# Kernel optimization log

Hardware: AMD Instinct MI355X
Metric: run time of the kernel (lower is better)

Reference implementation:

```python
import jax, jax.numpy as jnp
import numpy as np

B, N, D, T = 32, 512, 128, 8
NEG_SLOPE = 0.2
MASK_VAL = -1e10


def _xavier(key, shape, gain=1.0):
    fan_in, fan_out = shape[0], int(np.prod(shape[1:]))
    limit = gain * np.sqrt(6.0 / (fan_in + fan_out))
    return jax.random.uniform(key, shape, jnp.float32, -limit, limit)


def setup_inputs() -> dict:
    key = jax.random.key(0)
    ks = jax.random.split(key, 8)
    atom_embeddings = jax.random.normal(ks[0], (B, N, D), dtype=jnp.float32)
    # bond types in [-1, T-1]; -1 = no bond (masked)
    edges = jax.random.randint(ks[1], (B, N, N), 0, T + 1, dtype=jnp.int64) - 1
    Qw = _xavier(ks[2], (D, D))
    Kw = _xavier(ks[3], (D, D))
    Vw = _xavier(ks[4], (D, D))
    Pw = _xavier(ks[5], (D, D))
    Qb = jnp.zeros((D,), jnp.float32)
    Kb = jnp.zeros((D,), jnp.float32)
    Vb = jnp.zeros((D,), jnp.float32)
    Pb = jnp.zeros((D,), jnp.float32)
    a = _xavier(ks[6], (D, D, T), gain=1.414)
    return {"atom_embeddings": atom_embeddings, "edges": edges,
            "Qw": Qw, "Qb": Qb, "Kw": Kw, "Kb": Kb, "Vw": Vw, "Vb": Vb,
            "a": a, "Pw": Pw, "Pb": Pb}


def reference(atom_embeddings, edges, Qw, Qb, Kw, Kb, Vw, Vb, a, Pw, Pb):
    # torch Linear: x @ W.T + b
    src = atom_embeddings @ Qw.T + Qb            # (B,N,D)
    dst = atom_embeddings @ Kw.T + Kb            # (B,N,D)
    val = atom_embeddings @ Vw.T + Vb            # (B,N,D)

    # bilinear edge-type scores: s[b,n,m,t] = src[b,n,:] @ a[:,:,t] @ dst[b,m,:]
    ts = jnp.einsum('bnd,det->bnet', src, a)     # (B,N,D,T)
    scores = jnp.einsum('bnet,bme->bnmt', ts, dst)  # (B,N,N,T)

    # gather the slice for each edge's bond type (clamp -1 -> 0 like torch)
    idx = jnp.clip(edges, 0, None)[..., None]    # (B,N,N,1)
    att = jnp.take_along_axis(scores, idx, axis=-1)[..., 0]  # (B,N,N)
    att = jnp.where(edges == -1, MASK_VAL, att)
    att = jnp.where(att >= 0, att, NEG_SLOPE * att)  # leaky_relu
    att = jax.nn.softmax(att, axis=-1)           # (B,N,N)

    out = att @ val                              # (B,N,D)
    return out @ Pw.T + Pb
```

## Files before the change

kernel.cpp:

```cpp
#include <hip/hip_runtime.h>
#include <stdint.h>


typedef short bf16x8 __attribute__((ext_vector_type(8)));
typedef float f32x4 __attribute__((ext_vector_type(4)));
typedef unsigned short u16;
typedef unsigned int u32;

__device__ __forceinline__ u16 f2bf(float x) {
    union { float f; u32 u; } v; v.f = x;
    u32 r = v.u + 0x7FFFu + ((v.u >> 16) & 1u);
    return (u16)(r >> 16);
}
__device__ __forceinline__ float bf2f(u16 h) {
    union { u32 u; float f; } v; v.u = ((u32)h) << 16; return v.f;
}
__device__ __forceinline__ void split_hl(float x, u16& h, u16& l) {
    h = f2bf(x);
    l = f2bf(x - bf2f(h));
}
__device__ __forceinline__ f32x4 mfma16(bf16x8 a, bf16x8 b, f32x4 c) {
    return __builtin_amdgcn_mfma_f32_16x16x32_bf16(a, b, c, 0, 0, 0);
}

__global__ void prep_kernel(const float* __restrict__ Qw, const float* __restrict__ Qb,
                            const float* __restrict__ Kw, const float* __restrict__ Kb,
                            const float* __restrict__ Vw, const float* __restrict__ Vb,
                            const float* __restrict__ Aa, const float* __restrict__ Pw,
                            u16* __restrict__ WH, u16* __restrict__ WL,
                            float* __restrict__ bcat) {
    int gid = blockIdx.x * 256 + threadIdx.x;
    if (gid >= 1280 * 128) return;
    int j = gid >> 7, d = gid & 127;
    float v, bias = 0.f;
    if (j < 128) { v = Kw[j * 128 + d]; bias = Kb[j]; }
    else if (j < 256) {
        int jj = j - 128;
        float s = 0.f, bs = 0.f;
        for (int k = 0; k < 128; k++) {
            float p = Pw[jj * 128 + k];
            s += p * Vw[k * 128 + d];
            bs += p * Vb[k];
        }
        v = s; bias = bs;
    } else {
        int r = j - 256, t = r >> 7, jj = r & 127;
        float s = 0.f, bs = 0.f;
        for (int e = 0; e < 128; e++) {
            float av = Aa[(e * 128 + jj) * 8 + t];
            s += Qw[e * 128 + d] * av;
            bs += Qb[e] * av;
        }
        v = s; bias = bs;
    }
    u16 h, l; split_hl(v, h, l);
    WH[gid] = h; WL[gid] = l;
    if (d == 0) bcat[j] = bias;
}

__global__ void detect_kernel(const int* __restrict__ E, int* __restrict__ flag) {
    __shared__ int bad;
    if (threadIdx.x == 0) bad = 0;
    __syncthreads();
    int w0 = E[2 * threadIdx.x + 1];
    int w1 = E[2 * (threadIdx.x + 256) + 1];
    if (!(w0 == 0 || w0 == -1) || !(w1 == 0 || w1 == -1)) atomicOr(&bad, 1);
    __syncthreads();
    if (threadIdx.x == 0) *flag = (bad ? 0 : 1);
}

__global__ void econv_kernel(const void* __restrict__ E, const int* __restrict__ flag,
                             signed char* __restrict__ E8) {
    int i = (blockIdx.x * 256 + threadIdx.x) * 4;
    char4 o;
    if (*flag) {
        const long long* p = (const long long*)E;
        o.x = (signed char)p[i]; o.y = (signed char)p[i + 1];
        o.z = (signed char)p[i + 2]; o.w = (signed char)p[i + 3];
    } else {
        const int* p = (const int*)E;
        o.x = (signed char)p[i]; o.y = (signed char)p[i + 1];
        o.z = (signed char)p[i + 2]; o.w = (signed char)p[i + 3];
    }
    *(char4*)(E8 + i) = o;
}

__launch_bounds__(256, 2)
__global__ void gemm1_kernel(const float* __restrict__ X,
                             const u16* __restrict__ WH, const u16* __restrict__ WL,
                             const float* __restrict__ bcat,
                             u16* __restrict__ CH, u16* __restrict__ CL,
                             u16* __restrict__ VTH, u16* __restrict__ VTL) {
    const int id = blockIdx.x;
    const int xcd = id & 7, q5 = id >> 3;
    const int g = xcd * 32 + q5 / 20;
    const int jt = q5 - (q5 / 20) * 20;
    const int j0 = jt * 64;
    const int g0 = g * 64;
    __shared__ u16 AH[64 * 128], AL[64 * 128], BH[64 * 128], BL[64 * 128];
    const int tid = threadIdx.x;
    {
        const float4* Xv = (const float4*)(X + (size_t)g0 * 128);
        #pragma unroll
        for (int i = 0; i < 8; i++) {
            int idx = tid + i * 256;
            float4 x = Xv[idx];
            int row = idx >> 5, c4 = idx & 31;
            int boff = (row * 256 + c4 * 8) ^ ((row & 7) << 4);
            u16* ph = (u16*)((char*)AH + boff);
            u16* pl = (u16*)((char*)AL + boff);
            const float* xf = (const float*)&x;
            #pragma unroll
            for (int q = 0; q < 4; q++) { u16 h, l; split_hl(xf[q], h, l); ph[q] = h; pl[q] = l; }
        }
        const uint4* bh = (const uint4*)(WH + (size_t)j0 * 128);
        const uint4* bl = (const uint4*)(WL + (size_t)j0 * 128);
        #pragma unroll
        for (int i = 0; i < 4; i++) {
            int idx = tid + i * 256;
            int row = idx >> 4, ch = idx & 15;
            int boff = (row * 256 + ch * 16) ^ ((row & 7) << 4);
            *(uint4*)((char*)BH + boff) = bh[idx];
            *(uint4*)((char*)BL + boff) = bl[idx];
        }
    }
    __syncthreads();
    const int wid = tid >> 6, lane = tid & 63;
    const int wr = (wid >> 1) * 32, wc = (wid & 1) * 32;
    const int lr = lane & 15, lg = lane >> 4;
    f32x4 acc[2][2] = {};
    #pragma unroll
    for (int ks = 0; ks < 4; ks++) {
        const int kb2 = (ks * 32 + lg * 8) * 2;
        bf16x8 afh[2], afl[2], bfh[2], bfl[2];
        #pragma unroll
        for (int r = 0; r < 2; r++) {
            int row = wr + r * 16 + lr;
            int boff = (row * 256 + kb2) ^ ((row & 7) << 4);
            afh[r] = *(const bf16x8*)((const char*)AH + boff);
            afl[r] = *(const bf16x8*)((const char*)AL + boff);
        }
        #pragma unroll
        for (int c = 0; c < 2; c++) {
            int row = wc + c * 16 + lr;
            int boff = (row * 256 + kb2) ^ ((row & 7) << 4);
            bfh[c] = *(const bf16x8*)((const char*)BH + boff);
            bfl[c] = *(const bf16x8*)((const char*)BL + boff);
        }
        #pragma unroll
        for (int r = 0; r < 2; r++)
        #pragma unroll
        for (int c = 0; c < 2; c++) {
            acc[r][c] = mfma16(afh[r], bfh[c], acc[r][c]);
            acc[r][c] = mfma16(afh[r], bfl[c], acc[r][c]);
            acc[r][c] = mfma16(afl[r], bfh[c], acc[r][c]);
        }
    }
    const bool valTile = (j0 >= 128 && j0 < 256);
    #pragma unroll
    for (int r = 0; r < 2; r++)
    #pragma unroll
    for (int c = 0; c < 2; c++) {
        int j = j0 + wc + c * 16 + lr;
        float bias = bcat[j];
        #pragma unroll
        for (int q = 0; q < 4; q++) {
            int g1 = g0 + wr + r * 16 + 4 * lg + q;
            float v = acc[r][c][q] + bias;
            u16 h, l; split_hl(v, h, l);
            if (valTile) {
                int bb = g1 >> 9, n = g1 & 511;
                size_t off = ((size_t)(bb * 128 + (j - 128))) * 512 + n;
                VTH[off] = h; VTL[off] = l;
            } else {
                size_t off = (size_t)g1 * 1280 + j;
                CH[off] = h; CL[off] = l;
            }
        }
    }
}

__launch_bounds__(512, 2)
__global__ void scores_kernel(const u16* __restrict__ CH, const u16* __restrict__ CL,
                              const signed char* __restrict__ E8,
                              float* __restrict__ att) {
    const int id = blockIdx.x;
    const int xcd = id & 7, j = id >> 3;
    const int m0 = (j & 3) * 128;
    const int pair = xcd * 32 + (j >> 2);
    const int n0 = (pair & 7) * 64, b = pair >> 3;
    __shared__ u16 BH[128 * 128], BL[128 * 128];
    __shared__ u16 AH[2][64 * 128], AL[2][64 * 128];
    const int tid = threadIdx.x;
    const int wid = tid >> 6, lane = tid & 63;
    const int wr = (wid >> 2) * 32, wc = (wid & 3) * 32;
    const int lr = lane & 15, lg = lane >> 4;

    #pragma unroll
    for (int i = 0; i < 4; i++) {
        int idx = tid + i * 512;
        int row = idx >> 4, ch = idx & 15;
        size_t src = (size_t)(b * 512 + m0 + row) * 1280;
        int boff = (row * 256 + ch * 16) ^ ((row & 7) << 4);
        *(uint4*)((char*)BH + boff) = ((const uint4*)(CH + src))[ch];
        *(uint4*)((char*)BL + boff) = ((const uint4*)(CL + src))[ch];
    }
    int ed[2][2][4];
    #pragma unroll
    for (int r = 0; r < 2; r++)
    #pragma unroll
    for (int c = 0; c < 2; c++)
    #pragma unroll
    for (int q = 0; q < 4; q++) {
        int n = n0 + wr + r * 16 + 4 * lg + q;
        int m = m0 + wc + c * 16 + lr;
        ed[r][c][q] = E8[((size_t)b * 512 + n) * 512 + m];
    }
    uint4 rh[2], rl[2];
    {
        #pragma unroll
        for (int i = 0; i < 2; i++) {
            int idx = tid + i * 512;
            int row = idx >> 4, ch = idx & 15;
            size_t src = (size_t)(b * 512 + n0 + row) * 1280 + 256;
            rh[i] = ((const uint4*)(CH + src))[ch];
            rl[i] = ((const uint4*)(CL + src))[ch];
        }
        #pragma unroll
        for (int i = 0; i < 2; i++) {
            int idx = tid + i * 512;
            int row = idx >> 4, ch = idx & 15;
            int boff = (row * 256 + ch * 16) ^ ((row & 7) << 4);
            *(uint4*)((char*)AH[0] + boff) = rh[i];
            *(uint4*)((char*)AL[0] + boff) = rl[i];
        }
    }
    __syncthreads();
    bf16x8 bfh[4][2], bfl[4][2];
    #pragma unroll
    for (int ks = 0; ks < 4; ks++) {
        const int kb2 = (ks * 32 + lg * 8) * 2;
        #pragma unroll
        for (int c = 0; c < 2; c++) {
            int row = wc + c * 16 + lr;
            int boff = (row * 256 + kb2) ^ ((row & 7) << 4);
            bfh[ks][c] = *(const bf16x8*)((const char*)BH + boff);
            bfl[ks][c] = *(const bf16x8*)((const char*)BL + boff);
        }
    }
    float sel[2][2][4];
    #pragma unroll
    for (int r = 0; r < 2; r++)
    #pragma unroll
    for (int c = 0; c < 2; c++)
    #pragma unroll
    for (int q = 0; q < 4; q++) sel[r][c][q] = 0.f;

    for (int t = 0; t < 8; t++) {
        const int cur = t & 1;
        uint4 nh[2], nl[2];
        if (t < 7) {
            #pragma unroll
            for (int i = 0; i < 2; i++) {
                int idx = tid + i * 512;
                int row = idx >> 4, ch = idx & 15;
                size_t src = (size_t)(b * 512 + n0 + row) * 1280 + 256 + (t + 1) * 128;
                nh[i] = ((const uint4*)(CH + src))[ch];
                nl[i] = ((const uint4*)(CL + src))[ch];
            }
        }
        f32x4 acc[2][2] = {};
        #pragma unroll
        for (int ks = 0; ks < 4; ks++) {
            const int kb2 = (ks * 32 + lg * 8) * 2;
            bf16x8 afh[2], afl[2];
            #pragma unroll
            for (int r = 0; r < 2; r++) {
                int row = wr + r * 16 + lr;
                int boff = (row * 256 + kb2) ^ ((row & 7) << 4);
                afh[r] = *(const bf16x8*)((const char*)AH[cur] + boff);
                afl[r] = *(const bf16x8*)((const char*)AL[cur] + boff);
            }
            #pragma unroll
            for (int r = 0; r < 2; r++)
            #pragma unroll
            for (int c = 0; c < 2; c++) {
                acc[r][c] = mfma16(afh[r], bfh[ks][c], acc[r][c]);
                acc[r][c] = mfma16(afh[r], bfl[ks][c], acc[r][c]);
                acc[r][c] = mfma16(afl[r], bfh[ks][c], acc[r][c]);
            }
        }
        #pragma unroll
        for (int r = 0; r < 2; r++)
        #pragma unroll
        for (int c = 0; c < 2; c++)
        #pragma unroll
        for (int q = 0; q < 4; q++) {
            int ec = ed[r][c][q] < 0 ? 0 : ed[r][c][q];
            sel[r][c][q] = (ec == t) ? acc[r][c][q] : sel[r][c][q];
        }
        if (t < 7) {
            #pragma unroll
            for (int i = 0; i < 2; i++) {
                int idx = tid + i * 512;
                int row = idx >> 4, ch = idx & 15;
                int boff = (row * 256 + ch * 16) ^ ((row & 7) << 4);
                *(uint4*)((char*)AH[cur ^ 1] + boff) = nh[i];
                *(uint4*)((char*)AL[cur ^ 1] + boff) = nl[i];
            }
        }
        __syncthreads();
    }
    #pragma unroll
    for (int r = 0; r < 2; r++)
    #pragma unroll
    for (int c = 0; c < 2; c++)
    #pragma unroll
    for (int q = 0; q < 4; q++) {
        float v = (ed[r][c][q] == -1) ? -1e10f : sel[r][c][q];
        v = (v >= 0.f) ? v : 0.2f * v;
        size_t n = n0 + wr + r * 16 + 4 * lg + q;
        size_t m = m0 + wc + c * 16 + lr;
        att[((size_t)b * 512 + n) * 512 + m] = v;
    }
}

__launch_bounds__(256, 4)
__global__ void out_kernel(const float* __restrict__ att,
                           const u16* __restrict__ VTH, const u16* __restrict__ VTL,
                           const float* __restrict__ Pb, float* __restrict__ out) {
    const int id = blockIdx.x;
    const int xcd = id & 7, j = id >> 3;
    const int b = xcd * 4 + (j >> 4);
    const int n0 = (j & 15) * 32;
    __shared__ u16 PH[32 * 64], PL[32 * 64];
    __shared__ u16 VH[128 * 64], VL[128 * 64];
    __shared__ float smx[32], sinv[32];
    const int tid = threadIdx.x;
    const int wid = tid >> 6, lane = tid & 63;
    #pragma unroll
    for (int rr = 0; rr < 8; rr++) {
        int row = wid * 8 + rr;
        const float* rp = att + ((size_t)b * 512 + n0 + row) * 512;
        float4 a0 = ((const float4*)rp)[lane * 2];
        float4 a1 = ((const float4*)rp)[lane * 2 + 1];
        float mx = fmaxf(fmaxf(fmaxf(a0.x, a0.y), fmaxf(a0.z, a0.w)),
                         fmaxf(fmaxf(a1.x, a1.y), fmaxf(a1.z, a1.w)));
        #pragma unroll
        for (int o = 1; o < 64; o <<= 1) mx = fmaxf(mx, __shfl_xor(mx, o, 64));
        float s = expf(a0.x - mx) + expf(a0.y - mx) + expf(a0.z - mx) + expf(a0.w - mx)
                + expf(a1.x - mx) + expf(a1.y - mx) + expf(a1.z - mx) + expf(a1.w - mx);
        #pragma unroll
        for (int o = 1; o < 64; o <<= 1) s += __shfl_xor(s, o, 64);
        if (lane == 0) { smx[row] = mx; sinv[row] = 1.0f / s; }
    }
    __syncthreads();
    const int lr = lane & 15, lg = lane >> 4;
    const int wc = wid * 32;
    f32x4 acc[2][2] = {};
    for (int mc = 0; mc < 8; mc++) {
        {
            int row = tid >> 3, c8 = tid & 7;
            const float* rp = att + ((size_t)b * 512 + n0 + row) * 512 + mc * 64 + c8 * 8;
            float4 a0 = ((const float4*)rp)[0];
            float4 a1 = ((const float4*)rp)[1];
            float mxv = smx[row], iv = sinv[row];
            union { u16 us[8]; uint4 v; } uh, ul;
            float xs[8] = {a0.x, a0.y, a0.z, a0.w, a1.x, a1.y, a1.z, a1.w};
            #pragma unroll
            for (int q = 0; q < 8; q++) {
                float p = expf(xs[q] - mxv) * iv;
                split_hl(p, uh.us[q], ul.us[q]);
            }
            int boff = (row * 128 + c8 * 16) ^ ((row & 7) << 4);
            *(uint4*)((char*)PH + boff) = uh.v;
            *(uint4*)((char*)PL + boff) = ul.v;
        }
        #pragma unroll
        for (int i = 0; i < 4; i++) {
            int idx = tid + i * 256;
            int row = idx >> 3, ch = idx & 7;
            size_t src = ((size_t)(b * 128 + row)) * 512 + mc * 64;
            int boff = (row * 128 + ch * 16) ^ ((row & 7) << 4);
            *(uint4*)((char*)VH + boff) = ((const uint4*)(VTH + src))[ch];
            *(uint4*)((char*)VL + boff) = ((const uint4*)(VTL + src))[ch];
        }
        __syncthreads();
        #pragma unroll
        for (int ks = 0; ks < 2; ks++) {
            const int kb2 = (ks * 32 + lg * 8) * 2;
            bf16x8 ah[2], al[2];
            #pragma unroll
            for (int r = 0; r < 2; r++) {
                int row = r * 16 + lr;
                int boff = (row * 128 + kb2) ^ ((row & 7) << 4);
                ah[r] = *(const bf16x8*)((const char*)PH + boff);
                al[r] = *(const bf16x8*)((const char*)PL + boff);
            }
            #pragma unroll
            for (int c = 0; c < 2; c++) {
                int row = wc + c * 16 + lr;
                int boff = (row * 128 + kb2) ^ ((row & 7) << 4);
                bf16x8 bh = *(const bf16x8*)((const char*)VH + boff);
                bf16x8 bl = *(const bf16x8*)((const char*)VL + boff);
                #pragma unroll
                for (int r = 0; r < 2; r++) {
                    acc[r][c] = mfma16(ah[r], bh, acc[r][c]);
                    acc[r][c] = mfma16(ah[r], bl, acc[r][c]);
                    acc[r][c] = mfma16(al[r], bh, acc[r][c]);
                }
            }
        }
        __syncthreads();
    }
    #pragma unroll
    for (int r = 0; r < 2; r++)
    #pragma unroll
    for (int c = 0; c < 2; c++)
    #pragma unroll
    for (int q = 0; q < 4; q++) {
        int n = n0 + r * 16 + 4 * lg + q;
        int d = wc + c * 16 + lr;
        out[((size_t)b * 512 + n) * 128 + d] = acc[r][c][q] + Pb[d];
    }
}

extern "C" void kernel_launch(void* const* d_in, const int* in_sizes, int n_in,
                              void* d_out, int out_size, void* d_ws, size_t ws_size,
                              hipStream_t stream) {
    (void)in_sizes; (void)n_in; (void)out_size; (void)ws_size;
    const float* X  = (const float*)d_in[0];
    const void*  E  = d_in[1];
    const float* Qw = (const float*)d_in[2];
    const float* Qb = (const float*)d_in[3];
    const float* Kw = (const float*)d_in[4];
    const float* Kb = (const float*)d_in[5];
    const float* Vw = (const float*)d_in[6];
    const float* Vb = (const float*)d_in[7];
    const float* Aa = (const float*)d_in[8];
    const float* Pw = (const float*)d_in[9];
    const float* Pb = (const float*)d_in[10];
    float* out = (float*)d_out;

    char* ws = (char*)d_ws;
    size_t cur = 0;
    auto alloc = [&](size_t bytes) -> char* {
        char* p = ws + cur;
        cur += (bytes + 255) & ~(size_t)255;
        return p;
    };
    int*   flag = (int*)  alloc(4);
    u16*   WH   = (u16*)  alloc((size_t)1280 * 128 * 2);
    u16*   WL   = (u16*)  alloc((size_t)1280 * 128 * 2);
    float* bcat = (float*)alloc(1280 * 4);
    u16*   CH   = (u16*)  alloc((size_t)16384 * 1280 * 2);
    u16*   CL   = (u16*)  alloc((size_t)16384 * 1280 * 2);
    u16*   VTH  = (u16*)  alloc((size_t)32 * 128 * 512 * 2);
    u16*   VTL  = (u16*)  alloc((size_t)32 * 128 * 512 * 2);
    float* att  = (float*)alloc((size_t)32 * 512 * 512 * 4);
    signed char* E8 = (signed char*)alloc((size_t)32 * 512 * 512);

    prep_kernel<<<640, 256, 0, stream>>>(Qw, Qb, Kw, Kb, Vw, Vb, Aa, Pw, WH, WL, bcat);
    detect_kernel<<<1, 256, 0, stream>>>((const int*)E, flag);
    econv_kernel<<<8192, 256, 0, stream>>>(E, flag, E8);
    gemm1_kernel<<<5120, 256, 0, stream>>>(X, WH, WL, bcat, CH, CL, VTH, VTL);
    scores_kernel<<<1024, 512, 0, stream>>>(CH, CL, E8, att);
    out_kernel<<<512, 256, 0, stream>>>(att, VTH, VTL, Pb, out);
}
```

Measured before the change: 249.2 us.

## Reuse X tile across ten weight tiles in gemm1; single-pass softmax in out_kernel

gemm1 now launches 512 blocks, and each block keeps its 64-row X tile as bf16 fragments in registers while looping over 10 weight column tiles. Weight tiles are double-buffered in LDS, with the next tile prefetched through registers. This removes the repeated X loading and fp32-to-bf16 splitting that the old one-tile-per-block layout did. out_kernel now loads each attention row slice into registers once, computes max, exp and sum from those registers, and reuses the exp values for the P tiles, so att is read once instead of twice and exp is computed once instead of twice. In exchange both kernels use more registers and out_kernel's occupancy bound drops to 2, and gemm1's smaller grid may expose less parallelism.

```diff
diff --git a/kernel.cpp b/kernel.cpp
--- a/kernel.cpp
+++ b/kernel.cpp
@@ -93,12 +93,14 @@
                              u16* __restrict__ VTH, u16* __restrict__ VTL) {
     const int id = blockIdx.x;
     const int xcd = id & 7, q5 = id >> 3;
-    const int g = xcd * 32 + q5 / 20;
-    const int jt = q5 - (q5 / 20) * 20;
-    const int j0 = jt * 64;
-    const int g0 = g * 64;
-    __shared__ u16 AH[64 * 128], AL[64 * 128], BH[64 * 128], BL[64 * 128];
+    const int g0 = (xcd * 32 + (q5 >> 1)) * 64;
+    const int jbase = (q5 & 1) * 10;
+    __shared__ u16 WB[2][2][64 * 128];
     const int tid = threadIdx.x;
+    const int wid = tid >> 6, lane = tid & 63;
+    const int wr = (wid >> 1) * 32, wc = (wid & 1) * 32;
+    const int lr = lane & 15, lg = lane >> 4;
+
     {
         const float4* Xv = (const float4*)(X + (size_t)g0 * 128);
         #pragma unroll
@@ -107,74 +109,103 @@
             float4 x = Xv[idx];
             int row = idx >> 5, c4 = idx & 31;
             int boff = (row * 256 + c4 * 8) ^ ((row & 7) << 4);
-            u16* ph = (u16*)((char*)AH + boff);
-            u16* pl = (u16*)((char*)AL + boff);
+            u16* ph = (u16*)((char*)WB[1][0] + boff);
+            u16* pl = (u16*)((char*)WB[1][1] + boff);
             const float* xf = (const float*)&x;
             #pragma unroll
-            for (int q = 0; q < 4; q++) { u16 h, l; split_hl(xf[q], h, l); ph[q] = h; pl[q] = l; }
-        }
-        const uint4* bh = (const uint4*)(WH + (size_t)j0 * 128);
-        const uint4* bl = (const uint4*)(WL + (size_t)j0 * 128);
-        #pragma unroll
-        for (int i = 0; i < 4; i++) {
-            int idx = tid + i * 256;
-            int row = idx >> 4, ch = idx & 15;
-            int boff = (row * 256 + ch * 16) ^ ((row & 7) << 4);
-            *(uint4*)((char*)BH + boff) = bh[idx];
-            *(uint4*)((char*)BL + boff) = bl[idx];
-        }
+            for (int qq = 0; qq < 4; qq++) { u16 h, l; split_hl(xf[qq], h, l); ph[qq] = h; pl[qq] = l; }
+        }
+    }
+    uint4 nh[4], nl[4];
+    {
+        const uint4* bh = (const uint4*)(WH + (size_t)(jbase + 0) * 64 * 128);
+        const uint4* bl = (const uint4*)(WL + (size_t)(jbase + 0) * 64 * 128);
+        #pragma unroll
+        for (int i = 0; i < 4; i++) { nh[i] = bh[tid + i * 256]; nl[i] = bl[tid + i * 256]; }
     }
     __syncthreads();
-    const int wid = tid >> 6, lane = tid & 63;
-    const int wr = (wid >> 1) * 32, wc = (wid & 1) * 32;
-    const int lr = lane & 15, lg = lane >> 4;
-    f32x4 acc[2][2] = {};
+    bf16x8 afh[4][2], afl[4][2];
     #pragma unroll
     for (int ks = 0; ks < 4; ks++) {
         const int kb2 = (ks * 32 + lg * 8) * 2;
-        bf16x8 afh[2], afl[2], bfh[2], bfl[2];
         #pragma unroll
         for (int r = 0; r < 2; r++) {
             int row = wr + r * 16 + lr;
             int boff = (row * 256 + kb2) ^ ((row & 7) << 4);
-            afh[r] = *(const bf16x8*)((const char*)AH + boff);
-            afl[r] = *(const bf16x8*)((const char*)AL + boff);
-        }
+            afh[ks][r] = *(const bf16x8*)((const char*)WB[1][0] + boff);
+            afl[ks][r] = *(const bf16x8*)((const char*)WB[1][1] + boff);
+        }
+    }
+    #pragma unroll
+    for (int i = 0; i < 4; i++) {
+        int idx = tid + i * 256;
+        int row = idx >> 4, ch = idx & 15;
+        int boff = (row * 256 + ch * 16) ^ ((row & 7) << 4);
+        *(uint4*)((char*)WB[0][0] + boff) = nh[i];
+        *(uint4*)((char*)WB[0][1] + boff) = nl[i];
+    }
+
+    for (int jt = 0; jt < 10; jt++) {
+        __syncthreads();
+        if (jt < 9) {
+            const uint4* bh = (const uint4*)(WH + (size_t)(jbase + jt + 1) * 64 * 128);
+            const uint4* bl = (const uint4*)(WL + (size_t)(jbase + jt + 1) * 64 * 128);
+            #pragma unroll
+            for (int i = 0; i < 4; i++) { nh[i] = bh[tid + i * 256]; nl[i] = bl[tid + i * 256]; }
+        }
+        const int cur = jt & 1;
+        f32x4 acc[2][2] = {};
+        #pragma unroll
+        for (int ks = 0; ks < 4; ks++) {
+            const int kb2 = (ks * 32 + lg * 8) * 2;
+            bf16x8 bfh[2], bfl[2];
+            #pragma unroll
+            for (int c = 0; c < 2; c++) {
+                int row = wc + c * 16 + lr;
+                int boff = (row * 256 + kb2) ^ ((row & 7) << 4);
+                bfh[c] = *(const bf16x8*)((const char*)WB[cur][0] + boff);
+                bfl[c] = *(const bf16x8*)((const char*)WB[cur][1] + boff);
+            }
+            #pragma unroll
+            for (int r = 0; r < 2; r++)
+            #pragma unroll
+            for (int c = 0; c < 2; c++) {
+                acc[r][c] = mfma16(afh[ks][r], bfh[c], acc[r][c]);
+                acc[r][c] = mfma16(afh[ks][r], bfl[c], acc[r][c]);
+                acc[r][c] = mfma16(afl[ks][r], bfh[c], acc[r][c]);
+            }
+        }
+        const int j0 = (jbase + jt) * 64;
+        const bool valTile = (j0 >= 128 && j0 < 256);
+        #pragma unroll
+        for (int r = 0; r < 2; r++)
         #pragma unroll
         for (int c = 0; c < 2; c++) {
-            int row = wc + c * 16 + lr;
-            int boff = (row * 256 + kb2) ^ ((row & 7) << 4);
-            bfh[c] = *(const bf16x8*)((const char*)BH + boff);
-            bfl[c] = *(const bf16x8*)((const char*)BL + boff);
-        }
-        #pragma unroll
-        for (int r = 0; r < 2; r++)
-        #pragma unroll
-        for (int c = 0; c < 2; c++) {
-            acc[r][c] = mfma16(afh[r], bfh[c], acc[r][c]);
-            acc[r][c] = mfma16(afh[r], bfl[c], acc[r][c]);
-            acc[r][c] = mfma16(afl[r], bfh[c], acc[r][c]);
-        }
-    }
-    const bool valTile = (j0 >= 128 && j0 < 256);
-    #pragma unroll
-    for (int r = 0; r < 2; r++)
-    #pragma unroll
-    for (int c = 0; c < 2; c++) {
-        int j = j0 + wc + c * 16 + lr;
-        float bias = bcat[j];
-        #pragma unroll
-        for (int q = 0; q < 4; q++) {
-            int g1 = g0 + wr + r * 16 + 4 * lg + q;
-            float v = acc[r][c][q] + bias;
-            u16 h, l; split_hl(v, h, l);
-            if (valTile) {
-                int bb = g1 >> 9, n = g1 & 511;
-                size_t off = ((size_t)(bb * 128 + (j - 128))) * 512 + n;
-                VTH[off] = h; VTL[off] = l;
-            } else {
-                size_t off = (size_t)g1 * 1280 + j;
-                CH[off] = h; CL[off] = l;
+            int j = j0 + wc + c * 16 + lr;
+            float bias = bcat[j];
+            #pragma unroll
+            for (int qq = 0; qq < 4; qq++) {
+                int g1 = g0 + wr + r * 16 + 4 * lg + qq;
+                float v = acc[r][c][qq] + bias;
+                u16 h, l; split_hl(v, h, l);
+                if (valTile) {
+                    int bb = g1 >> 9, n = g1 & 511;
+                    size_t off = ((size_t)(bb * 128 + (j - 128))) * 512 + n;
+                    VTH[off] = h; VTL[off] = l;
+                } else {
+                    size_t off = (size_t)g1 * 1280 + j;
+                    CH[off] = h; CL[off] = l;
+                }
+            }
+        }
+        if (jt < 9) {
+            #pragma unroll
+            for (int i = 0; i < 4; i++) {
+                int idx = tid + i * 256;
+                int row = idx >> 4, ch = idx & 15;
+                int boff = (row * 256 + ch * 16) ^ ((row & 7) << 4);
+                *(uint4*)((char*)WB[cur ^ 1][0] + boff) = nh[i];
+                *(uint4*)((char*)WB[cur ^ 1][1] + boff) = nl[i];
             }
         }
     }
@@ -325,7 +356,7 @@
     }
 }
 
-__launch_bounds__(256, 4)
+__launch_bounds__(256, 2)
 __global__ void out_kernel(const float* __restrict__ att,
                            const u16* __restrict__ VTH, const u16* __restrict__ VTL,
                            const float* __restrict__ Pb, float* __restrict__ out) {
@@ -335,43 +366,51 @@
     const int n0 = (j & 15) * 32;
     __shared__ u16 PH[32 * 64], PL[32 * 64];
     __shared__ u16 VH[128 * 64], VL[128 * 64];
-    __shared__ float smx[32], sinv[32];
     const int tid = threadIdx.x;
+    const int row = tid >> 3, c8 = tid & 7;
+    float4 av0[8], av1[8];
+    const float4* rp = (const float4*)(att + ((size_t)b * 512 + n0 + row) * 512);
+    #pragma unroll
+    for (int mc = 0; mc < 8; mc++) {
+        av0[mc] = rp[mc * 16 + c8 * 2];
+        av1[mc] = rp[mc * 16 + c8 * 2 + 1];
+    }
+    float mx = -1e30f;
+    #pragma unroll
+    for (int mc = 0; mc < 8; mc++) {
+        mx = fmaxf(mx, fmaxf(fmaxf(fmaxf(av0[mc].x, av0[mc].y), fmaxf(av0[mc].z, av0[mc].w)),
+                             fmaxf(fmaxf(av1[mc].x, av1[mc].y), fmaxf(av1[mc].z, av1[mc].w))));
+    }
+    #pragma unroll
+    for (int o = 1; o < 8; o <<= 1) mx = fmaxf(mx, __shfl_xor(mx, o, 64));
+    float s = 0.f;
+    #pragma unroll
+    for (int mc = 0; mc < 8; mc++) {
+        av0[mc].x = expf(av0[mc].x - mx); av0[mc].y = expf(av0[mc].y - mx);
+        av0[mc].z = expf(av0[mc].z - mx); av0[mc].w = expf(av0[mc].w - mx);
+        av1[mc].x = expf(av1[mc].x - mx); av1[mc].y = expf(av1[mc].y - mx);
+        av1[mc].z = expf(av1[mc].z - mx); av1[mc].w = expf(av1[mc].w - mx);
+        s += av0[mc].x + av0[mc].y + av0[mc].z + av0[mc].w
+           + av1[mc].x + av1[mc].y + av1[mc].z + av1[mc].w;
+    }
+    #pragma unroll
+    for (int o = 1; o < 8; o <<= 1) s += __shfl_xor(s, o, 64);
+    const float inv = 1.0f / s;
     const int wid = tid >> 6, lane = tid & 63;
-    #pragma unroll
-    for (int rr = 0; rr < 8; rr++) {
-        int row = wid * 8 + rr;
-        const float* rp = att + ((size_t)b * 512 + n0 + row) * 512;
-        float4 a0 = ((const float4*)rp)[lane * 2];
-        float4 a1 = ((const float4*)rp)[lane * 2 + 1];
-        float mx = fmaxf(fmaxf(fmaxf(a0.x, a0.y), fmaxf(a0.z, a0.w)),
-                         fmaxf(fmaxf(a1.x, a1.y), fmaxf(a1.z, a1.w)));
-        #pragma unroll
-        for (int o = 1; o < 64; o <<= 1) mx = fmaxf(mx, __shfl_xor(mx, o, 64));
-        float s = expf(a0.x - mx) + expf(a0.y - mx) + expf(a0.z - mx) + expf(a0.w - mx)
-                + expf(a1.x - mx) + expf(a1.y - mx) + expf(a1.z - mx) + expf(a1.w - mx);
-        #pragma unroll
-        for (int o = 1; o < 64; o <<= 1) s += __shfl_xor(s, o, 64);
-        if (lane == 0) { smx[row] = mx; sinv[row] = 1.0f / s; }
-    }
-    __syncthreads();
     const int lr = lane & 15, lg = lane >> 4;
     const int wc = wid * 32;
     f32x4 acc[2][2] = {};
     for (int mc = 0; mc < 8; mc++) {
         {
-            int row = tid >> 3, c8 = tid & 7;
-            const float* rp = att + ((size_t)b * 512 + n0 + row) * 512 + mc * 64 + c8 * 8;
-            float4 a0 = ((const float4*)rp)[0];
-            float4 a1 = ((const float4*)rp)[1];
-            float mxv = smx[row], iv = sinv[row];
             union { u16 us[8]; uint4 v; } uh, ul;
-            float xs[8] = {a0.x, a0.y, a0.z, a0.w, a1.x, a1.y, a1.z, a1.w};
-            #pragma unroll
-            for (int q = 0; q < 8; q++) {
-                float p = expf(xs[q] - mxv) * iv;
-                split_hl(p, uh.us[q], ul.us[q]);
-            }
+            float xs0 = av0[mc].x * inv, xs1 = av0[mc].y * inv;
+            float xs2 = av0[mc].z * inv, xs3 = av0[mc].w * inv;
+            float xs4 = av1[mc].x * inv, xs5 = av1[mc].y * inv;
+            float xs6 = av1[mc].z * inv, xs7 = av1[mc].w * inv;
+            split_hl(xs0, uh.us[0], ul.us[0]); split_hl(xs1, uh.us[1], ul.us[1]);
+            split_hl(xs2, uh.us[2], ul.us[2]); split_hl(xs3, uh.us[3], ul.us[3]);
+            split_hl(xs4, uh.us[4], ul.us[4]); split_hl(xs5, uh.us[5], ul.us[5]);
+            split_hl(xs6, uh.us[6], ul.us[6]); split_hl(xs7, uh.us[7], ul.us[7]);
             int boff = (row * 128 + c8 * 16) ^ ((row & 7) << 4);
             *(uint4*)((char*)PH + boff) = uh.v;
             *(uint4*)((char*)PL + boff) = ul.v;
@@ -379,9 +418,9 @@
         #pragma unroll
         for (int i = 0; i < 4; i++) {
             int idx = tid + i * 256;
-            int row = idx >> 3, ch = idx & 7;
-            size_t src = ((size_t)(b * 128 + row)) * 512 + mc * 64;
-            int boff = (row * 128 + ch * 16) ^ ((row & 7) << 4);
+            int vrow = idx >> 3, ch = idx & 7;
+            size_t src = ((size_t)(b * 128 + vrow)) * 512 + mc * 64;
+            int boff = (vrow * 128 + ch * 16) ^ ((vrow & 7) << 4);
             *(uint4*)((char*)VH + boff) = ((const uint4*)(VTH + src))[ch];
             *(uint4*)((char*)VL + boff) = ((const uint4*)(VTL + src))[ch];
         }
@@ -392,15 +431,15 @@
             bf16x8 ah[2], al[2];
             #pragma unroll
             for (int r = 0; r < 2; r++) {
-                int row = r * 16 + lr;
-                int boff = (row * 128 + kb2) ^ ((row & 7) << 4);
+                int prow = r * 16 + lr;
+                int boff = (prow * 128 + kb2) ^ ((prow & 7) << 4);
                 ah[r] = *(const bf16x8*)((const char*)PH + boff);
                 al[r] = *(const bf16x8*)((const char*)PL + boff);
             }
             #pragma unroll
             for (int c = 0; c < 2; c++) {
-                int row = wc + c * 16 + lr;
-                int boff = (row * 128 + kb2) ^ ((row & 7) << 4);
+                int vrow = wc + c * 16 + lr;
+                int boff = (vrow * 128 + kb2) ^ ((vrow & 7) << 4);
                 bf16x8 bh = *(const bf16x8*)((const char*)VH + boff);
                 bf16x8 bl = *(const bf16x8*)((const char*)VL + boff);
                 #pragma unroll
@@ -463,7 +502,7 @@
     prep_kernel<<<640, 256, 0, stream>>>(Qw, Qb, Kw, Kb, Vw, Vb, Aa, Pw, WH, WL, bcat);
     detect_kernel<<<1, 256, 0, stream>>>((const int*)E, flag);
     econv_kernel<<<8192, 256, 0, stream>>>(E, flag, E8);
-    gemm1_kernel<<<5120, 256, 0, stream>>>(X, WH, WL, bcat, CH, CL, VTH, VTL);
+    gemm1_kernel<<<512, 256, 0, stream>>>(X, WH, WL, bcat, CH, CL, VTH, VTL);
     scores_kernel<<<1024, 512, 0, stream>>>(CH, CL, E8, att);
     out_kernel<<<512, 256, 0, stream>>>(att, VTH, VTL, Pb, out);
 }
```

New measurement: 250.2 us. No clear change (+0.4%).
